# Performance work log

Hardware: AMD Instinct MI355X
Metric: run time of the kernel (lower is better)

The kernel has to match this reference:

```python
import jax, jax.numpy as jnp
import numpy as np

B, H, K, HID = 64, 32, 4096, 7168
Q_LORA, KV_LORA = 1536, 512
NOPE, ROPE, VDIM = 128, 64, 128
HEAD_SIZE = NOPE + ROPE  # 192
EPS = 1e-6
SOFTMAX_SCALE = HEAD_SIZE ** -0.5  # mscale = 1 (no yarn)


def rmsnorm(x, w, eps=EPS):
    return x * jax.lax.rsqrt(jnp.mean(x * x, axis=-1, keepdims=True) + eps) * w


def interleave_rope(x, cos, sin):
    # x: [..., ROPE]; replicate torch view(d//2,2).transpose(2,3).reshape(d):
    # interleaved [r0,i0,r1,i1,...] -> [r0,r1,...,i0,i1,...], then rotate-half RoPE.
    shp = x.shape
    x = jnp.swapaxes(x.reshape(shp[:-1] + (ROPE // 2, 2)), -1, -2).reshape(shp)
    x1, x2 = x[..., : ROPE // 2], x[..., ROPE // 2:]
    # cos/sin: [B, ROPE//2] -> broadcast over head axis
    c = cos[:, None, :]
    s = sin[:, None, :]
    return jnp.concatenate([x1 * c - x2 * s, x2 * c + x1 * s], axis=-1)


def setup_inputs() -> dict:
    key = jax.random.key(0)
    ks = jax.random.split(key, 12)
    w = 0.02
    return {
        "hidden_states": jax.random.normal(ks[0], (B, HID), jnp.float32),
        "cos": jax.random.uniform(ks[1], (B, ROPE // 2), jnp.float32),
        "sin": jax.random.uniform(ks[2], (B, ROPE // 2), jnp.float32),
        "kv_cache": jax.random.normal(ks[3], (B, K, KV_LORA + ROPE), jnp.float32),
        "w_q_a": jax.random.normal(ks[4], (HID, Q_LORA), jnp.float32) * w,
        "q_a_ln_w": jnp.ones((Q_LORA,), jnp.float32),
        "w_q_b": jax.random.normal(ks[5], (Q_LORA, H * HEAD_SIZE), jnp.float32) * w,
        "w_kv_a": jax.random.normal(ks[6], (HID, KV_LORA + ROPE), jnp.float32) * w,
        "kv_a_ln_w": jnp.ones((KV_LORA,), jnp.float32),
        "w_uk_t": jax.random.normal(ks[7], (H, NOPE, KV_LORA), jnp.float32) * w,
        "w_uv": jax.random.normal(ks[8], (H, KV_LORA, VDIM), jnp.float32) * w,
        "w_o": jax.random.normal(ks[9], (H * VDIM, HID), jnp.float32) * w,
        "slots": jnp.full((B,), K - 1, jnp.int32),
        "seq_lens": jnp.full((B,), K, jnp.int32),
    }


def reference(hidden_states, cos, sin, kv_cache, w_q_a, q_a_ln_w, w_q_b,
              w_kv_a, kv_a_ln_w, w_uk_t, w_uv, w_o, slots, seq_lens):
    # --- Q low-rank path: q_a_proj -> RMSNorm -> q_b_proj ---
    q_c = rmsnorm(hidden_states @ w_q_a, q_a_ln_w)          # [B, Q_LORA]
    q = (q_c @ w_q_b).reshape(B, H, HEAD_SIZE)              # [B, H, 192]
    q_nope, q_pe = q[..., :NOPE], q[..., NOPE:]

    # --- K-up absorption: ql_nope = q_nope @ W_UK_T (per head) ---
    ql_nope = jnp.einsum("bhn,hnr->bhr", q_nope, w_uk_t)    # [B, H, KV_LORA]

    # --- compressed KV projection ---
    ckv = hidden_states @ w_kv_a                            # [B, KV_LORA+ROPE]
    kv_c, k_pe = ckv[:, :KV_LORA], ckv[:, KV_LORA:]
    kv_c = rmsnorm(kv_c, kv_a_ln_w)                         # [B, KV_LORA]
    k_pe = k_pe[:, None, :]                                 # [B, 1, ROPE]

    # --- interleaved RoPE on pe parts ---
    q_pe = interleave_rope(q_pe, cos, sin)                  # [B, H, ROPE]
    k_pe = interleave_rope(k_pe, cos, sin)[:, 0, :]         # [B, ROPE]

    # --- latent cache writeback ---
    latent_k = jnp.concatenate([kv_c, k_pe], axis=-1)       # [B, KV_LORA+ROPE]
    cache = kv_cache.at[jnp.arange(B), slots].set(latent_k)  # [B, K, 576]

    # --- MLA latent attention (decode) ---
    query = jnp.concatenate([ql_nope, q_pe], axis=-1)       # [B, H, 576]
    scores = jnp.einsum("bhd,bkd->bhk", query, cache) * SOFTMAX_SCALE
    valid = (jnp.arange(K)[None, :] < seq_lens[:, None])[:, None, :]  # [B,1,K]
    scores = jnp.where(valid, scores, jnp.finfo(scores.dtype).min)
    probs = jax.nn.softmax(scores, axis=-1)                 # [B, H, K]
    attn = jnp.einsum("bhk,bkr->bhr", probs, cache[..., :KV_LORA])  # [B,H,KV_LORA]

    # --- V-up absorption + output projection ---
    out = jnp.einsum("bhr,hrv->bhv", attn, w_uv)            # [B, H, VDIM]
    return out.reshape(B, H * VDIM) @ w_o                   # [B, HID]
```

## Files before the change

kernel.cpp:

```cpp
#include <hip/hip_runtime.h>
#include <stdint.h>

#define NB 64
#define NH 32
#define KCTX 4096
#define HID 7168
#define QLORA 1536
#define KVL 512
#define DTOT 576
#define NSPLIT 4
#define KSPAN 1024
#define NTILE 64
#define TK 16
#define SM_SCALE 0.07216878364870323f
#define NEGINF (-3.0e38f)

typedef __attribute__((ext_vector_type(4))) float f32x4;
typedef __attribute__((ext_vector_type(8))) __bf16 bf16x8;

#define LGKM_BARRIER() do{ asm volatile("s_waitcnt lgkmcnt(0)" ::: "memory"); __builtin_amdgcn_s_barrier(); } while(0)

static __device__ __forceinline__ void glds16(const void* g, void* s){
    __builtin_amdgcn_global_load_lds((const __attribute__((address_space(1))) void*)g,
                                     (__attribute__((address_space(3))) void*)s, 16, 0, 0);
}

static __device__ __forceinline__ unsigned short f2bf(float f){
    union{__bf16 h; unsigned short s;} x; x.h = (__bf16)f; return x.s;
}
static __device__ __forceinline__ float bf2f(unsigned short h){
    union{unsigned i;float f;}x; x.i=((unsigned)h)<<16; return x.f;
}
static __device__ __forceinline__ unsigned pack2(float a, float b){
    union{__bf16 h[2]; unsigned u;} x; x.h[0]=(__bf16)a; x.h[1]=(__bf16)b; return x.u;
}

__global__ __launch_bounds__(256) void pack_a(const float* __restrict__ A,
        unsigned short* __restrict__ Hi, unsigned short* __restrict__ Lo, int K)
{
    int idx = blockIdx.x*256 + threadIdx.x;
    int m = idx & 63, kb = idx >> 6;
    const float* src = A + (size_t)m*K + kb*8;
    float v[8];
    *(float4*)(v)   = *(const float4*)(src);
    *(float4*)(v+4) = *(const float4*)(src+4);
    unsigned short h[8], l[8];
#pragma unroll
    for (int j=0;j<8;++j){
        h[j] = f2bf(v[j]);
        l[j] = f2bf(v[j] - bf2f(h[j]));
    }
    uint4 uh, ul;
    uh.x=(unsigned)h[0]|((unsigned)h[1]<<16); uh.y=(unsigned)h[2]|((unsigned)h[3]<<16);
    uh.z=(unsigned)h[4]|((unsigned)h[5]<<16); uh.w=(unsigned)h[6]|((unsigned)h[7]<<16);
    ul.x=(unsigned)l[0]|((unsigned)l[1]<<16); ul.y=(unsigned)l[2]|((unsigned)l[3]<<16);
    ul.z=(unsigned)l[4]|((unsigned)l[5]<<16); ul.w=(unsigned)l[6]|((unsigned)l[7]<<16);
    *(uint4*)(Hi + (size_t)idx*8) = uh;
    *(uint4*)(Lo + (size_t)idx*8) = ul;
}

static __device__ __forceinline__ void gemm_core(
        const unsigned short* __restrict__ Ahi, const unsigned short* __restrict__ Alo,
        const float* __restrict__ Wm, float* __restrict__ P, int N, int ksteps,
        int bx, int by,
        unsigned short* Ah, unsigned short* Al, unsigned short* Bh, unsigned short* Bl)
{
    const int tid = threadIdx.x;
    const int w = tid>>6, l = tid&63, lm = l&15, lg = l>>4;
    const int n0 = bx*64;
    const int s  = by;
    const int mn = tid&63, ks = tid>>6;
    const int widx = ((mn>>4)*64 + ks*16 + (mn&15));

    f32x4 acc[4];
#pragma unroll
    for (int i=0;i<4;++i){ acc[i][0]=0.f; acc[i][1]=0.f; acc[i][2]=0.f; acc[i][3]=0.f; }

    uint4 ah4, al4; float wv[8];
    auto load_raw = [&](int t){
        const int k0 = (s*ksteps + t)*32;
        size_t gidx = (size_t)((k0>>3) + ks)*64 + mn;
        ah4 = *(const uint4*)(Ahi + gidx*8);
        al4 = *(const uint4*)(Alo + gidx*8);
        const float* wp = Wm + (size_t)(k0 + ks*8)*N + n0 + mn;
#pragma unroll
        for (int j=0;j<8;++j) wv[j] = wp[(size_t)j*N];
    };
    auto cvt_write = [&](int buf){
        unsigned short h[8], lo[8];
#pragma unroll
        for (int j=0;j<8;++j){
            h[j]  = f2bf(wv[j]);
            lo[j] = f2bf(wv[j] - bf2f(h[j]));
        }
        uint4 bh4, bl4;
        bh4.x=(unsigned)h[0]|((unsigned)h[1]<<16); bh4.y=(unsigned)h[2]|((unsigned)h[3]<<16);
        bh4.z=(unsigned)h[4]|((unsigned)h[5]<<16); bh4.w=(unsigned)h[6]|((unsigned)h[7]<<16);
        bl4.x=(unsigned)lo[0]|((unsigned)lo[1]<<16); bl4.y=(unsigned)lo[2]|((unsigned)lo[3]<<16);
        bl4.z=(unsigned)lo[4]|((unsigned)lo[5]<<16); bl4.w=(unsigned)lo[6]|((unsigned)lo[7]<<16);
        *(uint4*)(Ah + buf*2048 + widx*8) = ah4;
        *(uint4*)(Al + buf*2048 + widx*8) = al4;
        *(uint4*)(Bh + buf*2048 + widx*8) = bh4;
        *(uint4*)(Bl + buf*2048 + widx*8) = bl4;
    };

    load_raw(0);
    for (int t=0; t<ksteps; ++t){
        const int buf = t&1;
        cvt_write(buf);
        __syncthreads();
        if (t+1 < ksteps) load_raw(t+1);
        const int fa = buf*2048 + (w*64 + lg*16 + lm)*8;
        bf16x8 fah = *(const bf16x8*)(Ah + fa);
        bf16x8 fal = *(const bf16x8*)(Al + fa);
#pragma unroll
        for (int nt=0;nt<4;++nt){
            const int fb = buf*2048 + (nt*64 + lg*16 + lm)*8;
            bf16x8 fbh = *(const bf16x8*)(Bh + fb);
            bf16x8 fbl = *(const bf16x8*)(Bl + fb);
            acc[nt] = __builtin_amdgcn_mfma_f32_16x16x32_bf16(fah, fbh, acc[nt], 0,0,0);
            acc[nt] = __builtin_amdgcn_mfma_f32_16x16x32_bf16(fal, fbh, acc[nt], 0,0,0);
            acc[nt] = __builtin_amdgcn_mfma_f32_16x16x32_bf16(fah, fbl, acc[nt], 0,0,0);
        }
        __syncthreads();
    }
#pragma unroll
    for (int nt=0;nt<4;++nt){
        int n = n0 + nt*16 + lm;
#pragma unroll
        for (int r=0;r<4;++r){
            int m = w*16 + lg*4 + r;
            P[((size_t)s*64 + m)*N + n] = acc[nt][r];
        }
    }
}

__global__ __launch_bounds__(256) void gemm_mfma(
        const unsigned short* __restrict__ Ahi, const unsigned short* __restrict__ Alo,
        const float* __restrict__ Wm, float* __restrict__ P, int N, int ksteps)
{
    __shared__ unsigned short Ah[2*2048], Al[2*2048], Bh[2*2048], Bl[2*2048];
    gemm_core(Ahi, Alo, Wm, P, N, ksteps, blockIdx.x, blockIdx.y, Ah, Al, Bh, Bl);
}

__global__ __launch_bounds__(256) void gemm_dual(
        const unsigned short* __restrict__ Ahi, const unsigned short* __restrict__ Alo,
        const float* __restrict__ W0, float* __restrict__ P0, int N0, int ks0, int nbx0, int nblk0,
        const float* __restrict__ W1, float* __restrict__ P1, int N1, int ks1, int nbx1)
{
    __shared__ unsigned short Ah[2*2048], Al[2*2048], Bh[2*2048], Bl[2*2048];
    int bid = blockIdx.x;
    if (bid < nblk0){
        gemm_core(Ahi, Alo, W0, P0, N0, ks0, bid%nbx0, bid/nbx0, Ah, Al, Bh, Bl);
    } else {
        bid -= nblk0;
        gemm_core(Ahi, Alo, W1, P1, N1, ks1, bid%nbx1, bid/nbx1, Ah, Al, Bh, Bl);
    }
}

static __device__ __forceinline__ void rms_core(const float* __restrict__ P,
        const float* __restrict__ w, unsigned short* __restrict__ Hi,
        unsigned short* __restrict__ Lo, int S, int b, float* red)
{
    const int t = threadIdx.x;
    float v[6]; float ss = 0.f;
#pragma unroll
    for (int j=0;j<6;++j){
        int n = j*256 + t;
        float s = 0.f;
        for (int sp=0; sp<S; ++sp) s += P[((size_t)sp*64+b)*1536 + n];
        v[j] = s; ss += s*s;
    }
#pragma unroll
    for (int off=32; off>=1; off>>=1) ss += __shfl_xor(ss, off, 64);
    if ((t&63)==0) red[t>>6] = ss;
    __syncthreads();
    float tot = red[0]+red[1]+red[2]+red[3];
    float rs = rsqrtf(tot/1536.f + 1e-6f);
#pragma unroll
    for (int j=0;j<6;++j){
        int n = j*256+t;
        float val = v[j]*rs*w[n];
        unsigned short hs = f2bf(val);
        unsigned short ls = f2bf(val - bf2f(hs));
        size_t ui = (size_t)(n>>3)*512 + b*8 + (n&7);
        Hi[ui] = hs; Lo[ui] = ls;
    }
}

static __device__ __forceinline__ void kvrope_core(const float* __restrict__ P,
        const float* __restrict__ w, const float* __restrict__ cosb, const float* __restrict__ sinb,
        float* __restrict__ latent, int S, int b, float* vals, float* red)
{
    const int t = threadIdx.x;
    float ss = 0.f;
    for (int j=0;j<3;++j){
        int n = j*256+t;
        if (n < 576){
            float s=0.f;
            for (int sp=0;sp<S;++sp) s += P[((size_t)sp*64+b)*576 + n];
            vals[n]=s;
            if (n<512) ss += s*s;
        }
    }
#pragma unroll
    for (int off=32; off>=1; off>>=1) ss += __shfl_xor(ss, off, 64);
    if ((t&63)==0) red[t>>6]=ss;
    __syncthreads();
    float tot = red[0]+red[1]+red[2]+red[3];
    float rs = rsqrtf(tot/512.f + 1e-6f);
    for (int j=0;j<3;++j){
        int n = j*256+t;
        if (n<576){
            float o;
            if (n < 512) o = vals[n]*rs*w[n];
            else if (n < 544){ int i=n-512; o = vals[512+2*i]*cosb[b*32+i] - vals[513+2*i]*sinb[b*32+i]; }
            else            { int i=n-544; o = vals[513+2*i]*cosb[b*32+i] + vals[512+2*i]*sinb[b*32+i]; }
            latent[(size_t)b*576 + n] = o;
        }
    }
}

__global__ __launch_bounds__(256) void norm_dual(
        const float* __restrict__ Pq, const float* __restrict__ qw,
        unsigned short* __restrict__ Hi, unsigned short* __restrict__ Lo, int Sq,
        const float* __restrict__ Pkv, const float* __restrict__ kvw,
        const float* __restrict__ cosb, const float* __restrict__ sinb,
        float* __restrict__ latent, int Skv)
{
    __shared__ float vals[576];
    __shared__ float red[4];
    if (blockIdx.x < 64) rms_core(Pq, qw, Hi, Lo, Sq, blockIdx.x, red);
    else                 kvrope_core(Pkv, kvw, cosb, sinb, latent, Skv, blockIdx.x-64, vals, red);
}

__global__ __launch_bounds__(256) void reduce_sum(const float* __restrict__ P,
        float* __restrict__ out, int S, int N)
{
    int i = blockIdx.x*256 + threadIdx.x;
    int b = i / N, n = i - b*N;
    float s = 0.f;
    for (int sp=0; sp<S; ++sp) s += P[((size_t)sp*64+b)*N + n];
    out[i] = s;
}

__global__ __launch_bounds__(256) void finish_q(const float* __restrict__ P,
        const float* __restrict__ cosb, const float* __restrict__ sinb,
        float* __restrict__ q, float* __restrict__ query, int S)
{
    int i = blockIdx.x*256 + threadIdx.x;
    int b = i / 6144, n = i - b*6144;
    float s = 0.f;
    for (int sp=0; sp<S; ++sp) s += P[((size_t)sp*64+b)*6144 + n];
    int h = n/192, nl = n - h*192;
    if (nl < 128){
        q[((size_t)b*32+h)*192 + nl] = s;
    } else {
        int i2 = (nl-128)>>1;
        float other = __shfl_xor(s, 1);
        float c = cosb[b*32+i2], sn = sinb[b*32+i2];
        float* o = query + ((size_t)b*32+h)*576;
        if ((nl&1)==0) o[512+i2] = s*c - other*sn;
        else           o[544+i2] = s*c + other*sn;
    }
}

__global__ __launch_bounds__(256) void qlnope_mfma(const float* __restrict__ q,
        const float* __restrict__ wukt, float* __restrict__ query)
{
    __shared__ unsigned short Bh[4096], Bl[4096];
    const int h = blockIdx.x, r0 = blockIdx.y*128;
    const int tid = threadIdx.x;
    const int w = tid>>6, l = tid&63, lm = l&15, lg = l>>4;
    f32x4 acc[8];
#pragma unroll
    for (int i=0;i<8;++i){ acc[i][0]=0.f; acc[i][1]=0.f; acc[i][2]=0.f; acc[i][3]=0.f; }

    for (int ck=0; ck<4; ++ck){
        const int k0 = ck*32;
        unsigned short hh[2][8], ll[2][8]; int wid0 = tid*2;
#pragma unroll
        for (int wi=0; wi<2; ++wi){
            int wid = wid0 + wi;
            int ntile = wid>>6, kg = (wid>>4)&3, nl = wid&15;
            int n = r0 + ntile*16 + nl;
            const float* wp = wukt + (size_t)h*65536 + (size_t)(k0+kg*8)*512 + n;
#pragma unroll
            for (int j=0;j<8;++j){
                float v = wp[(size_t)j*512];
                hh[wi][j] = f2bf(v);
                ll[wi][j] = f2bf(v - bf2f(hh[wi][j]));
            }
        }
        __syncthreads();
#pragma unroll
        for (int wi=0; wi<2; ++wi){
            int wid = wid0 + wi;
            uint4 uh, ul;
            uh.x=(unsigned)hh[wi][0]|((unsigned)hh[wi][1]<<16); uh.y=(unsigned)hh[wi][2]|((unsigned)hh[wi][3]<<16);
            uh.z=(unsigned)hh[wi][4]|((unsigned)hh[wi][5]<<16); uh.w=(unsigned)hh[wi][6]|((unsigned)hh[wi][7]<<16);
            ul.x=(unsigned)ll[wi][0]|((unsigned)ll[wi][1]<<16); ul.y=(unsigned)ll[wi][2]|((unsigned)ll[wi][3]<<16);
            ul.z=(unsigned)ll[wi][4]|((unsigned)ll[wi][5]<<16); ul.w=(unsigned)ll[wi][6]|((unsigned)ll[wi][7]<<16);
            *(uint4*)(Bh + wid*8) = uh;
            *(uint4*)(Bl + wid*8) = ul;
        }
        __syncthreads();
        const int bb = w*16 + lm;
        const float* ap = q + ((size_t)bb*32 + h)*192 + k0 + lg*8;
        float4 a0 = *(const float4*)ap;
        float4 a1 = *(const float4*)(ap+4);
        union{uint4 u; bf16x8 v;} fh, fl;
        fh.u.x=pack2(a0.x,a0.y); fh.u.y=pack2(a0.z,a0.w);
        fh.u.z=pack2(a1.x,a1.y); fh.u.w=pack2(a1.z,a1.w);
        float r0f=a0.x-bf2f(f2bf(a0.x)), r1f=a0.y-bf2f(f2bf(a0.y));
        float r2f=a0.z-bf2f(f2bf(a0.z)), r3f=a0.w-bf2f(f2bf(a0.w));
        float r4f=a1.x-bf2f(f2bf(a1.x)), r5f=a1.y-bf2f(f2bf(a1.y));
        float r6f=a1.z-bf2f(f2bf(a1.z)), r7f=a1.w-bf2f(f2bf(a1.w));
        fl.u.x=pack2(r0f,r1f); fl.u.y=pack2(r2f,r3f);
        fl.u.z=pack2(r4f,r5f); fl.u.w=pack2(r6f,r7f);
#pragma unroll
        for (int nt=0;nt<8;++nt){
            const int fb = (nt*64 + lg*16 + lm)*8;
            bf16x8 fbh = *(const bf16x8*)(Bh + fb);
            bf16x8 fbl = *(const bf16x8*)(Bl + fb);
            acc[nt] = __builtin_amdgcn_mfma_f32_16x16x32_bf16(fh.v, fbh, acc[nt], 0,0,0);
            acc[nt] = __builtin_amdgcn_mfma_f32_16x16x32_bf16(fl.v, fbh, acc[nt], 0,0,0);
            acc[nt] = __builtin_amdgcn_mfma_f32_16x16x32_bf16(fh.v, fbl, acc[nt], 0,0,0);
        }
        __syncthreads();
    }
#pragma unroll
    for (int nt=0;nt<8;++nt){
        int r = r0 + nt*16 + lm;
#pragma unroll
        for (int qq=0;qq<4;++qq){
            int bb = w*16 + lg*4 + qq;
            query[((size_t)bb*32 + h)*576 + r] = acc[nt][qq];
        }
    }
}

static __device__ __forceinline__ int vt_addr(int d, int key){
    return (d>>2)*64 + (((d&3)^((d>>3)&3))<<4) + key;
}

__global__ __launch_bounds__(256,1) void attn_mfma(const float* __restrict__ query,
        const float* __restrict__ kv, const float* __restrict__ latent,
        const int* __restrict__ slots, const int* __restrict__ seq_lens,
        float* __restrict__ Opart, float* __restrict__ Mpart, float* __restrict__ Lpart)
{
    __shared__ float Kf[3][16*576];
    __shared__ unsigned short Vt[8192];
    __shared__ float S_s[2][32][16];
    __shared__ unsigned short P_s[32][40];
    __shared__ float alpha_s[32];

    const int b = blockIdx.y, sp = blockIdx.x;
    const int tid = threadIdx.x;
    const int w = tid>>6, l = tid&63;
    const int lm = l&15, lg = l>>4;
    const int ht = w&1;
    const int dh = w>>1;
    const int seqlen = seq_lens[b];
    const int slot = slots[b];
    const int k0 = sp*KSPAN;
    const int myh = tid>>3, s5 = tid&7;

    {
        int id = tid*2;
        P_s[id>>4][16 + (id&15)] = 0;
        id++;
        P_s[id>>4][16 + (id&15)] = 0;
    }

    bf16x8 qf[9];
    {
        const float* qrow = query + ((size_t)b*32 + ht*16 + lm)*576;
#pragma unroll
        for (int ss=0;ss<9;++ss){
            int d0 = (dh*9+ss)*32 + lg*8;
            float4 a = *(const float4*)(qrow + d0);
            float4 c = *(const float4*)(qrow + d0 + 4);
            union{uint4 u; bf16x8 v;} cv;
            cv.u.x=pack2(a.x,a.y); cv.u.y=pack2(a.z,a.w);
            cv.u.z=pack2(c.x,c.y); cv.u.w=pack2(c.z,c.w);
            qf[ss]=cv.v;
        }
    }

    auto issue_tile = [&](int tt, int buf){
        const int gkb = k0 + tt*TK;
#pragma unroll
        for (int i=0;i<9;++i){
            int B = w*9216 + i*1024 + l*16;
            int r = B / 2304;
            int gs = (B - r*2304) >> 4;
            int g  = gs ^ (r&7);
            int gk = gkb + r; if (gk > KCTX-1) gk = KCTX-1;
            const float* src = (gk==slot) ? (latent + (size_t)b*576 + g*4)
                                          : (kv + ((size_t)b*KCTX + gk)*576 + g*4);
            glds16(src, ((char*)&Kf[buf][0]) + w*9216 + i*1024);
        }
    };

    f32x4 oacc[16];
#pragma unroll
    for (int i=0;i<16;++i){ oacc[i][0]=0.f; oacc[i][1]=0.f; oacc[i][2]=0.f; oacc[i][3]=0.f; }
    float m_run = NEGINF, l_run = 0.f;

    issue_tile(0, 0);
    issue_tile(1, 1);
    asm volatile("s_waitcnt vmcnt(9)" ::: "memory");
    __builtin_amdgcn_s_barrier();

    int cur = 0;
    for (int tt=0; tt<NTILE; ++tt){
        if (tt+2 < NTILE){
            int ib = cur+2; if (ib>=3) ib-=3;
            issue_tile(tt+2, ib);
        }

        {
            const int kg = tid&1;
            const int dq = tid>>1;
            float4 rv[8];
#pragma unroll
            for (int i=0;i<8;++i){
                int r = kg*8 + i;
                rv[i] = *(const float4*)(&Kf[cur][r*576 + ((dq ^ (r&7))<<2)]);
            }
#pragma unroll
            for (int j=0;j<4;++j){
                const float* f0 = (const float*)&rv[0];
                const float* f1 = (const float*)&rv[1];
                const float* f2 = (const float*)&rv[2];
                const float* f3 = (const float*)&rv[3];
                const float* f4 = (const float*)&rv[4];
                const float* f5 = (const float*)&rv[5];
                const float* f6 = (const float*)&rv[6];
                const float* f7 = (const float*)&rv[7];
                uint4 o;
                o.x = pack2(f0[j], f1[j]); o.y = pack2(f2[j], f3[j]);
                o.z = pack2(f4[j], f5[j]); o.w = pack2(f6[j], f7[j]);
                *(uint4*)(Vt + vt_addr(dq*4+j, kg*8)) = o;
            }
        }
        {
            f32x4 sacc; sacc[0]=0.f; sacc[1]=0.f; sacc[2]=0.f; sacc[3]=0.f;
            const float* kb = &Kf[cur][lm*576];
            const int sw = lm&7;
            __builtin_amdgcn_s_setprio(1);
#pragma unroll
            for (int ss=0;ss<9;++ss){
                int g = dh*72 + ss*8 + lg*2;
                float4 fa = *(const float4*)(kb + ((g ^ sw)<<2));
                float4 fb = *(const float4*)(kb + (((g+1) ^ sw)<<2));
                union{uint4 u; bf16x8 v;} cv;
                cv.u.x = pack2(fa.x, fa.y); cv.u.y = pack2(fa.z, fa.w);
                cv.u.z = pack2(fb.x, fb.y); cv.u.w = pack2(fb.z, fb.w);
                sacc = __builtin_amdgcn_mfma_f32_16x16x32_bf16(qf[ss], cv.v, sacc, 0,0,0);
            }
            __builtin_amdgcn_s_setprio(0);
#pragma unroll
            for (int r=0;r<4;++r) S_s[dh][ht*16 + (lg<<2) + r][lm] = sacc[r];
        }
        LGKM_BARRIER();

        {
            const int kbase = k0 + tt*TK;
            float sc[2];
#pragma unroll
            for (int j=0;j<2;++j){
                int k = s5 + 8*j;
                float v = (S_s[0][myh][k] + S_s[1][myh][k])*SM_SCALE;
                sc[j] = (kbase + k < seqlen) ? v : NEGINF;
            }
            float tmax = fmaxf(sc[0],sc[1]);
            tmax = fmaxf(tmax, __shfl_xor(tmax,1));
            tmax = fmaxf(tmax, __shfl_xor(tmax,2));
            tmax = fmaxf(tmax, __shfl_xor(tmax,4));
            float mnew = fmaxf(m_run, tmax);
            float al = __expf(m_run - mnew);
            float ps = 0.f;
#pragma unroll
            for (int j=0;j<2;++j){
                float pv = (sc[j] > 0.5f*NEGINF) ? __expf(sc[j]-mnew) : 0.f;
                ps += pv;
                P_s[myh][s5 + 8*j] = f2bf(pv);
            }
            ps += __shfl_xor(ps,1); ps += __shfl_xor(ps,2); ps += __shfl_xor(ps,4);
            l_run = l_run*al + ps;
            m_run = mnew;
            if (s5==0) alpha_s[myh] = al;
        }
        LGKM_BARRIER();

        {
            float al4[4];
#pragma unroll
            for (int r=0;r<4;++r) al4[r] = alpha_s[ht*16 + (lg<<2) + r];
            bf16x8 pa = *(const bf16x8*)(&P_s[ht*16+lm][lg*8]);
            __builtin_amdgcn_s_setprio(1);
#pragma unroll
            for (int nt=0;nt<16;++nt){
                f32x4 o = oacc[nt];
                o[0]*=al4[0]; o[1]*=al4[1]; o[2]*=al4[2]; o[3]*=al4[3];
                int r = dh*256 + nt*16 + lm;
                bf16x8 bv = *(const bf16x8*)(Vt + vt_addr(r, (lg&1)*8));
                oacc[nt] = __builtin_amdgcn_mfma_f32_16x16x32_bf16(pa, bv, o, 0,0,0);
            }
            __builtin_amdgcn_s_setprio(0);
        }
        if (tt+2 < NTILE){
            asm volatile("s_waitcnt vmcnt(9)" ::: "memory");
            __builtin_amdgcn_s_barrier();
        } else if (tt+1 < NTILE){
            asm volatile("s_waitcnt vmcnt(0)" ::: "memory");
            __builtin_amdgcn_s_barrier();
        }
        cur = cur+1; if (cur>=3) cur-=3;
    }

    const int obase = (b*NSPLIT+sp)*32;
#pragma unroll
    for (int nt=0;nt<16;++nt){
        int r = dh*256 + nt*16 + lm;
#pragma unroll
        for (int qq=0;qq<4;++qq){
            int h = ht*16 + (lg<<2) + qq;
            Opart[((size_t)(obase+h))*512 + r] = oacc[nt][qq];
        }
    }
    if (s5==0){ Mpart[obase+myh]=m_run; Lpart[obase+myh]=l_run; }
}

__global__ __launch_bounds__(256) void av_uv_merge(const float* __restrict__ Opart,
        const float* __restrict__ Mpart, const float* __restrict__ Lpart,
        const float* __restrict__ wuv,
        unsigned short* __restrict__ Hi, unsigned short* __restrict__ Lo)
{
    __shared__ unsigned short Bh[4096], Bl[4096];
    __shared__ float lwn[64][4];
    const int h = blockIdx.x;
    const int tid = threadIdx.x;
    const int w = tid>>6, l = tid&63, lm = l&15, lg = l>>4;

    if (tid < 64){
        int b = tid;
        float m0 = Mpart[(b*NSPLIT+0)*32+h], m1 = Mpart[(b*NSPLIT+1)*32+h];
        float m2 = Mpart[(b*NSPLIT+2)*32+h], m3 = Mpart[(b*NSPLIT+3)*32+h];
        float M = fmaxf(fmaxf(m0,m1),fmaxf(m2,m3));
        float w0 = __expf(m0-M), w1 = __expf(m1-M), w2 = __expf(m2-M), w3 = __expf(m3-M);
        float L = w0*Lpart[(b*NSPLIT+0)*32+h] + w1*Lpart[(b*NSPLIT+1)*32+h]
                + w2*Lpart[(b*NSPLIT+2)*32+h] + w3*Lpart[(b*NSPLIT+3)*32+h];
        float inv = 1.f/L;
        lwn[b][0]=w0*inv; lwn[b][1]=w1*inv; lwn[b][2]=w2*inv; lwn[b][3]=w3*inv;
    }
    __syncthreads();

    f32x4 acc[8];
#pragma unroll
    for (int i=0;i<8;++i){ acc[i][0]=0.f; acc[i][1]=0.f; acc[i][2]=0.f; acc[i][3]=0.f; }

    for (int ck=0; ck<16; ++ck){
        const int k0 = ck*32;
        unsigned short hh[2][8], ll[2][8]; int wid0 = tid*2;
#pragma unroll
        for (int wi=0; wi<2; ++wi){
            int wid = wid0 + wi;
            int ntile = wid>>6, kg = (wid>>4)&3, nl = wid&15;
            int n = ntile*16 + nl;
            const float* wp = wuv + (size_t)h*65536 + (size_t)(k0+kg*8)*128 + n;
#pragma unroll
            for (int j=0;j<8;++j){
                float v = wp[(size_t)j*128];
                hh[wi][j] = f2bf(v);
                ll[wi][j] = f2bf(v - bf2f(hh[wi][j]));
            }
        }
        __syncthreads();
#pragma unroll
        for (int wi=0; wi<2; ++wi){
            int wid = wid0 + wi;
            uint4 uh, ul;
            uh.x=(unsigned)hh[wi][0]|((unsigned)hh[wi][1]<<16); uh.y=(unsigned)hh[wi][2]|((unsigned)hh[wi][3]<<16);
            uh.z=(unsigned)hh[wi][4]|((unsigned)hh[wi][5]<<16); uh.w=(unsigned)hh[wi][6]|((unsigned)hh[wi][7]<<16);
            ul.x=(unsigned)ll[wi][0]|((unsigned)ll[wi][1]<<16); ul.y=(unsigned)ll[wi][2]|((unsigned)ll[wi][3]<<16);
            ul.z=(unsigned)ll[wi][4]|((unsigned)ll[wi][5]<<16); ul.w=(unsigned)ll[wi][6]|((unsigned)ll[wi][7]<<16);
            *(uint4*)(Bh + wid*8) = uh;
            *(uint4*)(Bl + wid*8) = ul;
        }
        __syncthreads();
        const int bb = w*16 + lm;
        const float* op = Opart + (((size_t)bb*NSPLIT)*32 + h)*512 + k0 + lg*8;
        float l0=lwn[bb][0], l1=lwn[bb][1], l2=lwn[bb][2], l3=lwn[bb][3];
        float4 s0a = *(const float4*)(op);          float4 s0b = *(const float4*)(op+4);
        float4 s1a = *(const float4*)(op+16384);    float4 s1b = *(const float4*)(op+16388);
        float4 s2a = *(const float4*)(op+32768);    float4 s2b = *(const float4*)(op+32772);
        float4 s3a = *(const float4*)(op+49152);    float4 s3b = *(const float4*)(op+49156);
        float a[8];
        a[0]=l0*s0a.x+l1*s1a.x+l2*s2a.x+l3*s3a.x;
        a[1]=l0*s0a.y+l1*s1a.y+l2*s2a.y+l3*s3a.y;
        a[2]=l0*s0a.z+l1*s1a.z+l2*s2a.z+l3*s3a.z;
        a[3]=l0*s0a.w+l1*s1a.w+l2*s2a.w+l3*s3a.w;
        a[4]=l0*s0b.x+l1*s1b.x+l2*s2b.x+l3*s3b.x;
        a[5]=l0*s0b.y+l1*s1b.y+l2*s2b.y+l3*s3b.y;
        a[6]=l0*s0b.z+l1*s1b.z+l2*s2b.z+l3*s3b.z;
        a[7]=l0*s0b.w+l1*s1b.w+l2*s2b.w+l3*s3b.w;
        union{uint4 u; bf16x8 v;} fh, fl;
        unsigned short hsv[8], lsv[8];
#pragma unroll
        for (int j=0;j<8;++j){ hsv[j]=f2bf(a[j]); lsv[j]=f2bf(a[j]-bf2f(hsv[j])); }
        fh.u.x=(unsigned)hsv[0]|((unsigned)hsv[1]<<16); fh.u.y=(unsigned)hsv[2]|((unsigned)hsv[3]<<16);
        fh.u.z=(unsigned)hsv[4]|((unsigned)hsv[5]<<16); fh.u.w=(unsigned)hsv[6]|((unsigned)hsv[7]<<16);
        fl.u.x=(unsigned)lsv[0]|((unsigned)lsv[1]<<16); fl.u.y=(unsigned)lsv[2]|((unsigned)lsv[3]<<16);
        fl.u.z=(unsigned)lsv[4]|((unsigned)lsv[5]<<16); fl.u.w=(unsigned)lsv[6]|((unsigned)lsv[7]<<16);
#pragma unroll
        for (int nt=0;nt<8;++nt){
            const int fb = (nt*64 + lg*16 + lm)*8;
            bf16x8 fbh = *(const bf16x8*)(Bh + fb);
            bf16x8 fbl = *(const bf16x8*)(Bl + fb);
            acc[nt] = __builtin_amdgcn_mfma_f32_16x16x32_bf16(fh.v, fbh, acc[nt], 0,0,0);
            acc[nt] = __builtin_amdgcn_mfma_f32_16x16x32_bf16(fl.v, fbh, acc[nt], 0,0,0);
            acc[nt] = __builtin_amdgcn_mfma_f32_16x16x32_bf16(fh.v, fbl, acc[nt], 0,0,0);
        }
        __syncthreads();
    }
#pragma unroll
    for (int nt=0;nt<8;++nt){
#pragma unroll
        for (int qq=0;qq<4;++qq){
            float val = acc[nt][qq];
            int bb = w*16 + lg*4 + qq;
            int k = h*128 + nt*16 + lm;
            unsigned short hv = f2bf(val);
            unsigned short lv = f2bf(val - bf2f(hv));
            size_t ui = (size_t)(k>>3)*512 + bb*8 + (k&7);
            Hi[ui] = hv; Lo[ui] = lv;
        }
    }
}

extern "C" void kernel_launch(void* const* d_in, const int* in_sizes, int n_in,
                              void* d_out, int out_size, void* d_ws, size_t ws_size,
                              hipStream_t stream)
{
    const float* hidden = (const float*)d_in[0];
    const float* cosb   = (const float*)d_in[1];
    const float* sinb   = (const float*)d_in[2];
    const float* kv     = (const float*)d_in[3];
    const float* w_q_a  = (const float*)d_in[4];
    const float* q_ln   = (const float*)d_in[5];
    const float* w_q_b  = (const float*)d_in[6];
    const float* w_kv_a = (const float*)d_in[7];
    const float* kv_ln  = (const float*)d_in[8];
    const float* w_uk_t = (const float*)d_in[9];
    const float* w_uv   = (const float*)d_in[10];
    const float* w_o    = (const float*)d_in[11];
    const int* slots    = (const int*)d_in[12];
    const int* seqlens  = (const int*)d_in[13];
    float* out = (float*)d_out;

    float* W = (float*)d_ws;
    float* P0     = W;
    float* P1     = W + 4194304;
    float* q      = W + 6291456;
    float* query  = W + 6684672;
    float* latent = W + 7864320;
    float* Mp     = W + 7901184;
    float* Lp     = W + 7909376;
    unsigned short* pkhid_h = (unsigned short*)(W + 7917568);
    unsigned short* pkhid_l = (unsigned short*)(W + 8146944);
    unsigned short* pkqc_h  = (unsigned short*)(W + 8376320);
    unsigned short* pkqc_l  = (unsigned short*)(W + 8425472);
    unsigned short* pkao_h  = (unsigned short*)(W + 8474624);
    unsigned short* pkao_l  = (unsigned short*)(W + 8605696);

    hipLaunchKernelGGL(pack_a, dim3(224), dim3(256), 0, stream, hidden, pkhid_h, pkhid_l, 7168);
    hipLaunchKernelGGL(gemm_dual, dim3(672+504), dim3(256), 0, stream,
                       pkhid_h, pkhid_l, w_q_a, P0, 1536, 8, 24, 672, w_kv_a, P1, 576, 4, 9);
    hipLaunchKernelGGL(norm_dual, dim3(128), dim3(256), 0, stream,
                       P0, q_ln, pkqc_h, pkqc_l, 28, P1, kv_ln, cosb, sinb, latent, 56);
    hipLaunchKernelGGL(gemm_mfma, dim3(96,6), dim3(256), 0, stream, pkqc_h, pkqc_l, w_q_b, P0, 6144, 8);
    hipLaunchKernelGGL(finish_q, dim3(1536), dim3(256), 0, stream, P0, cosb, sinb, q, query, 6);
    hipLaunchKernelGGL(qlnope_mfma, dim3(32,4), dim3(256), 0, stream, q, w_uk_t, query);
    hipLaunchKernelGGL(attn_mfma, dim3(NSPLIT,64), dim3(256), 0, stream,
                       query, kv, latent, slots, seqlens, P0, Mp, Lp);
    hipLaunchKernelGGL(av_uv_merge, dim3(32), dim3(256), 0, stream, P0, Mp, Lp, w_uv, pkao_h, pkao_l);
    hipLaunchKernelGGL(gemm_mfma, dim3(112,8), dim3(256), 0, stream, pkao_h, pkao_l, w_o, P0, 7168, 16);
    hipLaunchKernelGGL(reduce_sum, dim3(1792), dim3(256), 0, stream, P0, out, 8, 7168);
}
```

Baseline: 387.7 us.

## Double attention block width to 8 waves and split V-up merge across batch groups

The attention kernel moves from 4 to 8 waves per block. The 18 K-dimension chunks of QK^T are split unevenly across 4 wave pairs (4/5/5/4), V output columns are split 4 ways, and tile loads and V transposes are spread over more threads. This adds latency hiding and memory-level parallelism in the dominant streaming kernel, at the cost of extra partial-score reduction in shared memory and more register and barrier pressure. Separately, av_uv_merge gains a batch-group grid dimension (32x4 blocks) so it fills more compute units, though each block recomputes the w_uv hi/lo split.

Result: faster. 332.6 us (-14.2%).

```diff
diff --git a/kernel.cpp b/kernel.cpp
--- a/kernel.cpp
+++ b/kernel.cpp
@@ -344,14 +344,14 @@
     return (d>>2)*64 + (((d&3)^((d>>3)&3))<<4) + key;
 }
 
-__global__ __launch_bounds__(256,1) void attn_mfma(const float* __restrict__ query,
+__global__ __launch_bounds__(512,1) void attn_mfma(const float* __restrict__ query,
         const float* __restrict__ kv, const float* __restrict__ latent,
         const int* __restrict__ slots, const int* __restrict__ seq_lens,
         float* __restrict__ Opart, float* __restrict__ Mpart, float* __restrict__ Lpart)
 {
     __shared__ float Kf[3][16*576];
     __shared__ unsigned short Vt[8192];
-    __shared__ float S_s[2][32][16];
+    __shared__ float S_s[4][32][16];
     __shared__ unsigned short P_s[32][40];
     __shared__ float alpha_s[32];
 
@@ -360,57 +360,63 @@
     const int w = tid>>6, l = tid&63;
     const int lm = l&15, lg = l>>4;
     const int ht = w&1;
-    const int dh = w>>1;
+    const int dg = w>>1;
+    const int cs = dg*5 - (dg>0?1:0);
+    const int cnt = (dg==1||dg==2)?5:4;
     const int seqlen = seq_lens[b];
     const int slot = slots[b];
     const int k0 = sp*KSPAN;
-    const int myh = tid>>3, s5 = tid&7;
-
-    {
-        int id = tid*2;
-        P_s[id>>4][16 + (id&15)] = 0;
-        id++;
-        P_s[id>>4][16 + (id&15)] = 0;
-    }
-
-    bf16x8 qf[9];
+    const int myh = tid>>4, s5 = tid&15;
+
+    P_s[tid>>4][16 + (tid&15)] = 0;
+
+    bf16x8 qf[5];
     {
         const float* qrow = query + ((size_t)b*32 + ht*16 + lm)*576;
 #pragma unroll
-        for (int ss=0;ss<9;++ss){
-            int d0 = (dh*9+ss)*32 + lg*8;
-            float4 a = *(const float4*)(qrow + d0);
-            float4 c = *(const float4*)(qrow + d0 + 4);
-            union{uint4 u; bf16x8 v;} cv;
-            cv.u.x=pack2(a.x,a.y); cv.u.y=pack2(a.z,a.w);
-            cv.u.z=pack2(c.x,c.y); cv.u.w=pack2(c.z,c.w);
-            qf[ss]=cv.v;
+        for (int ss=0;ss<5;++ss){
+            if (ss < cnt){
+                int d0 = (cs+ss)*32 + lg*8;
+                float4 a = *(const float4*)(qrow + d0);
+                float4 c = *(const float4*)(qrow + d0 + 4);
+                union{uint4 u; bf16x8 v;} cv;
+                cv.u.x=pack2(a.x,a.y); cv.u.y=pack2(a.z,a.w);
+                cv.u.z=pack2(c.x,c.y); cv.u.w=pack2(c.z,c.w);
+                qf[ss]=cv.v;
+            } else {
+                union{uint4 u; bf16x8 v;} z; z.u.x=0; z.u.y=0; z.u.z=0; z.u.w=0;
+                qf[ss]=z.v;
+            }
         }
     }
 
     auto issue_tile = [&](int tt, int buf){
         const int gkb = k0 + tt*TK;
 #pragma unroll
-        for (int i=0;i<9;++i){
-            int B = w*9216 + i*1024 + l*16;
-            int r = B / 2304;
-            int gs = (B - r*2304) >> 4;
-            int g  = gs ^ (r&7);
-            int gk = gkb + r; if (gk > KCTX-1) gk = KCTX-1;
-            const float* src = (gk==slot) ? (latent + (size_t)b*576 + g*4)
-                                          : (kv + ((size_t)b*KCTX + gk)*576 + g*4);
-            glds16(src, ((char*)&Kf[buf][0]) + w*9216 + i*1024);
+        for (int i=0;i<5;++i){
+            int s = i*8 + w;
+            if (s < 36){
+                int B = s*1024 + l*16;
+                int r = B / 2304;
+                int gs = (B - r*2304) >> 4;
+                int g  = gs ^ (r&7);
+                int gk = gkb + r; if (gk > KCTX-1) gk = KCTX-1;
+                const float* src = (gk==slot) ? (latent + (size_t)b*576 + g*4)
+                                              : (kv + ((size_t)b*KCTX + gk)*576 + g*4);
+                glds16(src, ((char*)&Kf[buf][0]) + B);
+            }
         }
     };
 
-    f32x4 oacc[16];
-#pragma unroll
-    for (int i=0;i<16;++i){ oacc[i][0]=0.f; oacc[i][1]=0.f; oacc[i][2]=0.f; oacc[i][3]=0.f; }
+    f32x4 oacc[8];
+#pragma unroll
+    for (int i=0;i<8;++i){ oacc[i][0]=0.f; oacc[i][1]=0.f; oacc[i][2]=0.f; oacc[i][3]=0.f; }
     float m_run = NEGINF, l_run = 0.f;
 
     issue_tile(0, 0);
     issue_tile(1, 1);
-    asm volatile("s_waitcnt vmcnt(9)" ::: "memory");
+    if (w < 4) { asm volatile("s_waitcnt vmcnt(5)" ::: "memory"); }
+    else       { asm volatile("s_waitcnt vmcnt(4)" ::: "memory"); }
     __builtin_amdgcn_s_barrier();
 
     int cur = 0;
@@ -422,27 +428,20 @@
 
         {
             const int kg = tid&1;
-            const int dq = tid>>1;
-            float4 rv[8];
-#pragma unroll
-            for (int i=0;i<8;++i){
-                int r = kg*8 + i;
+            const int dq = (tid>>1)&127;
+            const int rep = tid>>8;
+            float4 rv[4];
+#pragma unroll
+            for (int i=0;i<4;++i){
+                int r = kg*8 + rep*4 + i;
                 rv[i] = *(const float4*)(&Kf[cur][r*576 + ((dq ^ (r&7))<<2)]);
             }
 #pragma unroll
             for (int j=0;j<4;++j){
-                const float* f0 = (const float*)&rv[0];
-                const float* f1 = (const float*)&rv[1];
-                const float* f2 = (const float*)&rv[2];
-                const float* f3 = (const float*)&rv[3];
-                const float* f4 = (const float*)&rv[4];
-                const float* f5 = (const float*)&rv[5];
-                const float* f6 = (const float*)&rv[6];
-                const float* f7 = (const float*)&rv[7];
-                uint4 o;
-                o.x = pack2(f0[j], f1[j]); o.y = pack2(f2[j], f3[j]);
-                o.z = pack2(f4[j], f5[j]); o.w = pack2(f6[j], f7[j]);
-                *(uint4*)(Vt + vt_addr(dq*4+j, kg*8)) = o;
+                uint2 o;
+                o.x = pack2(((const float*)&rv[0])[j], ((const float*)&rv[1])[j]);
+                o.y = pack2(((const float*)&rv[2])[j], ((const float*)&rv[3])[j]);
+                *(uint2*)(Vt + vt_addr(dq*4+j, kg*8) + rep*4) = o;
             }
         }
         {
@@ -451,8 +450,9 @@
             const int sw = lm&7;
             __builtin_amdgcn_s_setprio(1);
 #pragma unroll
-            for (int ss=0;ss<9;++ss){
-                int g = dh*72 + ss*8 + lg*2;
+            for (int ss=0;ss<5;++ss){
+                int chunk = cs + (ss<cnt ? ss : 0);
+                int g = chunk*8 + lg*2;
                 float4 fa = *(const float4*)(kb + ((g ^ sw)<<2));
                 float4 fb = *(const float4*)(kb + (((g+1) ^ sw)<<2));
                 union{uint4 u; bf16x8 v;} cv;
@@ -462,33 +462,27 @@
             }
             __builtin_amdgcn_s_setprio(0);
 #pragma unroll
-            for (int r=0;r<4;++r) S_s[dh][ht*16 + (lg<<2) + r][lm] = sacc[r];
+            for (int r=0;r<4;++r) S_s[dg][ht*16 + (lg<<2) + r][lm] = sacc[r];
         }
         LGKM_BARRIER();
 
         {
             const int kbase = k0 + tt*TK;
-            float sc[2];
-#pragma unroll
-            for (int j=0;j<2;++j){
-                int k = s5 + 8*j;
-                float v = (S_s[0][myh][k] + S_s[1][myh][k])*SM_SCALE;
-                sc[j] = (kbase + k < seqlen) ? v : NEGINF;
-            }
-            float tmax = fmaxf(sc[0],sc[1]);
+            float v = (S_s[0][myh][s5] + S_s[1][myh][s5]
+                     + S_s[2][myh][s5] + S_s[3][myh][s5])*SM_SCALE;
+            float sc = (kbase + s5 < seqlen) ? v : NEGINF;
+            float tmax = sc;
             tmax = fmaxf(tmax, __shfl_xor(tmax,1));
             tmax = fmaxf(tmax, __shfl_xor(tmax,2));
             tmax = fmaxf(tmax, __shfl_xor(tmax,4));
+            tmax = fmaxf(tmax, __shfl_xor(tmax,8));
             float mnew = fmaxf(m_run, tmax);
             float al = __expf(m_run - mnew);
-            float ps = 0.f;
-#pragma unroll
-            for (int j=0;j<2;++j){
-                float pv = (sc[j] > 0.5f*NEGINF) ? __expf(sc[j]-mnew) : 0.f;
-                ps += pv;
-                P_s[myh][s5 + 8*j] = f2bf(pv);
-            }
-            ps += __shfl_xor(ps,1); ps += __shfl_xor(ps,2); ps += __shfl_xor(ps,4);
+            float pv = (sc > 0.5f*NEGINF) ? __expf(sc-mnew) : 0.f;
+            P_s[myh][s5] = f2bf(pv);
+            float ps = pv;
+            ps += __shfl_xor(ps,1); ps += __shfl_xor(ps,2);
+            ps += __shfl_xor(ps,4); ps += __shfl_xor(ps,8);
             l_run = l_run*al + ps;
             m_run = mnew;
             if (s5==0) alpha_s[myh] = al;
@@ -502,17 +496,18 @@
             bf16x8 pa = *(const bf16x8*)(&P_s[ht*16+lm][lg*8]);
             __builtin_amdgcn_s_setprio(1);
 #pragma unroll
-            for (int nt=0;nt<16;++nt){
+            for (int nt=0;nt<8;++nt){
                 f32x4 o = oacc[nt];
                 o[0]*=al4[0]; o[1]*=al4[1]; o[2]*=al4[2]; o[3]*=al4[3];
-                int r = dh*256 + nt*16 + lm;
+                int r = dg*128 + nt*16 + lm;
                 bf16x8 bv = *(const bf16x8*)(Vt + vt_addr(r, (lg&1)*8));
                 oacc[nt] = __builtin_amdgcn_mfma_f32_16x16x32_bf16(pa, bv, o, 0,0,0);
             }
             __builtin_amdgcn_s_setprio(0);
         }
         if (tt+2 < NTILE){
-            asm volatile("s_waitcnt vmcnt(9)" ::: "memory");
+            if (w < 4) { asm volatile("s_waitcnt vmcnt(5)" ::: "memory"); }
+            else       { asm volatile("s_waitcnt vmcnt(4)" ::: "memory"); }
             __builtin_amdgcn_s_barrier();
         } else if (tt+1 < NTILE){
             asm volatile("s_waitcnt vmcnt(0)" ::: "memory");
@@ -523,8 +518,8 @@
 
     const int obase = (b*NSPLIT+sp)*32;
 #pragma unroll
-    for (int nt=0;nt<16;++nt){
-        int r = dh*256 + nt*16 + lm;
+    for (int nt=0;nt<8;++nt){
+        int r = dg*128 + nt*16 + lm;
 #pragma unroll
         for (int qq=0;qq<4;++qq){
             int h = ht*16 + (lg<<2) + qq;
@@ -540,13 +535,14 @@
         unsigned short* __restrict__ Hi, unsigned short* __restrict__ Lo)
 {
     __shared__ unsigned short Bh[4096], Bl[4096];
-    __shared__ float lwn[64][4];
-    const int h = blockIdx.x;
+    __shared__ unsigned short Ah[512], Al[512];
+    __shared__ float lwn[16][4];
+    const int h = blockIdx.x, bg = blockIdx.y;
     const int tid = threadIdx.x;
     const int w = tid>>6, l = tid&63, lm = l&15, lg = l>>4;
 
-    if (tid < 64){
-        int b = tid;
+    if (tid < 16){
+        int b = bg*16 + tid;
         float m0 = Mpart[(b*NSPLIT+0)*32+h], m1 = Mpart[(b*NSPLIT+1)*32+h];
         float m2 = Mpart[(b*NSPLIT+2)*32+h], m3 = Mpart[(b*NSPLIT+3)*32+h];
         float M = fmaxf(fmaxf(m0,m1),fmaxf(m2,m3));
@@ -554,13 +550,13 @@
         float L = w0*Lpart[(b*NSPLIT+0)*32+h] + w1*Lpart[(b*NSPLIT+1)*32+h]
                 + w2*Lpart[(b*NSPLIT+2)*32+h] + w3*Lpart[(b*NSPLIT+3)*32+h];
         float inv = 1.f/L;
-        lwn[b][0]=w0*inv; lwn[b][1]=w1*inv; lwn[b][2]=w2*inv; lwn[b][3]=w3*inv;
+        lwn[tid][0]=w0*inv; lwn[tid][1]=w1*inv; lwn[tid][2]=w2*inv; lwn[tid][3]=w3*inv;
     }
     __syncthreads();
 
-    f32x4 acc[8];
-#pragma unroll
-    for (int i=0;i<8;++i){ acc[i][0]=0.f; acc[i][1]=0.f; acc[i][2]=0.f; acc[i][3]=0.f; }
+    f32x4 acc[2];
+#pragma unroll
+    for (int i=0;i<2;++i){ acc[i][0]=0.f; acc[i][1]=0.f; acc[i][2]=0.f; acc[i][3]=0.f; }
 
     for (int ck=0; ck<16; ++ck){
         const int k0 = ck*32;
@@ -577,6 +573,16 @@
                 hh[wi][j] = f2bf(v);
                 ll[wi][j] = f2bf(v - bf2f(hh[wi][j]));
             }
+        }
+        float av[2];
+#pragma unroll
+        for (int e=0;e<2;++e){
+            int id = tid*2+e;
+            int row = id>>5, k = id&31;
+            int bb = bg*16 + row;
+            const float* op = Opart + (((size_t)bb*NSPLIT)*32 + h)*512 + k0 + k;
+            av[e] = lwn[row][0]*op[0] + lwn[row][1]*op[16384]
+                  + lwn[row][2]*op[32768] + lwn[row][3]*op[49152];
         }
         __syncthreads();
 #pragma unroll
@@ -590,48 +596,38 @@
             *(uint4*)(Bh + wid*8) = uh;
             *(uint4*)(Bl + wid*8) = ul;
         }
-        __syncthreads();
-        const int bb = w*16 + lm;
-        const float* op = Opart + (((size_t)bb*NSPLIT)*32 + h)*512 + k0 + lg*8;
-        float l0=lwn[bb][0], l1=lwn[bb][1], l2=lwn[bb][2], l3=lwn[bb][3];
-        float4 s0a = *(const float4*)(op);          float4 s0b = *(const float4*)(op+4);
-        float4 s1a = *(const float4*)(op+16384);    float4 s1b = *(const float4*)(op+16388);
-        float4 s2a = *(const float4*)(op+32768);    float4 s2b = *(const float4*)(op+32772);
-        float4 s3a = *(const float4*)(op+49152);    float4 s3b = *(const float4*)(op+49156);
-        float a[8];
-        a[0]=l0*s0a.x+l1*s1a.x+l2*s2a.x+l3*s3a.x;
-        a[1]=l0*s0a.y+l1*s1a.y+l2*s2a.y+l3*s3a.y;
-        a[2]=l0*s0a.z+l1*s1a.z+l2*s2a.z+l3*s3a.z;
-        a[3]=l0*s0a.w+l1*s1a.w+l2*s2a.w+l3*s3a.w;
-        a[4]=l0*s0b.x+l1*s1b.x+l2*s2b.x+l3*s3b.x;
-        a[5]=l0*s0b.y+l1*s1b.y+l2*s2b.y+l3*s3b.y;
-        a[6]=l0*s0b.z+l1*s1b.z+l2*s2b.z+l3*s3b.z;
-        a[7]=l0*s0b.w+l1*s1b.w+l2*s2b.w+l3*s3b.w;
-        union{uint4 u; bf16x8 v;} fh, fl;
-        unsigned short hsv[8], lsv[8];
-#pragma unroll
-        for (int j=0;j<8;++j){ hsv[j]=f2bf(a[j]); lsv[j]=f2bf(a[j]-bf2f(hsv[j])); }
-        fh.u.x=(unsigned)hsv[0]|((unsigned)hsv[1]<<16); fh.u.y=(unsigned)hsv[2]|((unsigned)hsv[3]<<16);
-        fh.u.z=(unsigned)hsv[4]|((unsigned)hsv[5]<<16); fh.u.w=(unsigned)hsv[6]|((unsigned)hsv[7]<<16);
-        fl.u.x=(unsigned)lsv[0]|((unsigned)lsv[1]<<16); fl.u.y=(unsigned)lsv[2]|((unsigned)lsv[3]<<16);
-        fl.u.z=(unsigned)lsv[4]|((unsigned)lsv[5]<<16); fl.u.w=(unsigned)lsv[6]|((unsigned)lsv[7]<<16);
-#pragma unroll
-        for (int nt=0;nt<8;++nt){
+#pragma unroll
+        for (int e=0;e<2;++e){
+            int id = tid*2+e;
+            int row = id>>5, k = id&31;
+            unsigned short hs = f2bf(av[e]);
+            unsigned short ls = f2bf(av[e] - bf2f(hs));
+            int ai = ((k>>3)*16 + row)*8 + (k&7);
+            Ah[ai] = hs; Al[ai] = ls;
+        }
+        __syncthreads();
+        const int fa = (lg*16 + lm)*8;
+        bf16x8 fah = *(const bf16x8*)(Ah + fa);
+        bf16x8 fal = *(const bf16x8*)(Al + fa);
+#pragma unroll
+        for (int i=0;i<2;++i){
+            int nt = w*2 + i;
             const int fb = (nt*64 + lg*16 + lm)*8;
             bf16x8 fbh = *(const bf16x8*)(Bh + fb);
             bf16x8 fbl = *(const bf16x8*)(Bl + fb);
-            acc[nt] = __builtin_amdgcn_mfma_f32_16x16x32_bf16(fh.v, fbh, acc[nt], 0,0,0);
-            acc[nt] = __builtin_amdgcn_mfma_f32_16x16x32_bf16(fl.v, fbh, acc[nt], 0,0,0);
-            acc[nt] = __builtin_amdgcn_mfma_f32_16x16x32_bf16(fh.v, fbl, acc[nt], 0,0,0);
-        }
-        __syncthreads();
-    }
-#pragma unroll
-    for (int nt=0;nt<8;++nt){
+            acc[i] = __builtin_amdgcn_mfma_f32_16x16x32_bf16(fah, fbh, acc[i], 0,0,0);
+            acc[i] = __builtin_amdgcn_mfma_f32_16x16x32_bf16(fal, fbh, acc[i], 0,0,0);
+            acc[i] = __builtin_amdgcn_mfma_f32_16x16x32_bf16(fah, fbl, acc[i], 0,0,0);
+        }
+        __syncthreads();
+    }
+#pragma unroll
+    for (int i=0;i<2;++i){
+        int nt = w*2 + i;
 #pragma unroll
         for (int qq=0;qq<4;++qq){
-            float val = acc[nt][qq];
-            int bb = w*16 + lg*4 + qq;
+            float val = acc[i][qq];
+            int bb = bg*16 + lg*4 + qq;
             int k = h*128 + nt*16 + lm;
             unsigned short hv = f2bf(val);
             unsigned short lv = f2bf(val - bf2f(hv));
@@ -684,9 +680,9 @@
     hipLaunchKernelGGL(gemm_mfma, dim3(96,6), dim3(256), 0, stream, pkqc_h, pkqc_l, w_q_b, P0, 6144, 8);
     hipLaunchKernelGGL(finish_q, dim3(1536), dim3(256), 0, stream, P0, cosb, sinb, q, query, 6);
     hipLaunchKernelGGL(qlnope_mfma, dim3(32,4), dim3(256), 0, stream, q, w_uk_t, query);
-    hipLaunchKernelGGL(attn_mfma, dim3(NSPLIT,64), dim3(256), 0, stream,
+    hipLaunchKernelGGL(attn_mfma, dim3(NSPLIT,64), dim3(512), 0, stream,
                        query, kv, latent, slots, seqlens, P0, Mp, Lp);
-    hipLaunchKernelGGL(av_uv_merge, dim3(32), dim3(256), 0, stream, P0, Mp, Lp, w_uv, pkao_h, pkao_l);
+    hipLaunchKernelGGL(av_uv_merge, dim3(32,4), dim3(256), 0, stream, P0, Mp, Lp, w_uv, pkao_h, pkao_l);
     hipLaunchKernelGGL(gemm_mfma, dim3(112,8), dim3(256), 0, stream, pkao_h, pkao_l, w_o, P0, 7168, 16);
     hipLaunchKernelGGL(reduce_sum, dim3(1792), dim3(256), 0, stream, P0, out, 8, 7168);
 }
```
